# Performance work log

Measured on AMD Instinct MI355X. Metric: run time of the kernel, lower is better.

The kernel has to match this reference:

```python
import jax, jax.numpy as jnp
import numpy as np

N_BITS = 4
QN = -(2 ** (N_BITS - 1))      # -8
QP = 2 ** (N_BITS - 1) - 1     # 7

IN_F, OUT_F, RANK, N_STEPS = 4096, 4096, 8, 10


def ste_qdq(x, scale):
    """LSQ-style quantize-dequantize (forward math of STEFunction, zero_point=0)."""
    v = x / scale
    q = jnp.clip(jnp.round(v), QN, QP)
    return q * scale


def setup_inputs() -> dict:
    key = jax.random.key(0)
    ks = jax.random.split(key, 4)
    x = jax.random.normal(ks[0], (4, 2048, IN_F), dtype=jnp.float32)
    pretrained_weight = jax.random.normal(ks[1], (OUT_F, IN_F), dtype=jnp.float32)
    lora_A = jax.random.normal(ks[2], (RANK, IN_F), dtype=jnp.float32) * 0.01
    lora_B = jnp.zeros((OUT_F, RANK), dtype=jnp.float32)
    weight_scale = jnp.ones((OUT_F,), dtype=jnp.float32) * 0.1
    temporal_scales = jnp.ones((N_STEPS,), dtype=jnp.float32) * 0.1
    bias = jnp.zeros((OUT_F,), dtype=jnp.float32)
    return {
        "x": x,
        "pretrained_weight": pretrained_weight,
        "lora_A": lora_A,
        "lora_B": lora_B,
        "weight_scale": weight_scale,
        "temporal_scales": temporal_scales,
        "bias": bias,
        "current_step": 0,
    }


def reference(x, pretrained_weight, lora_A, lora_B, weight_scale, temporal_scales, bias, current_step):
    # LoRA merge: [O,R] @ [R,I] -> [O,I]
    merged_weight = pretrained_weight + lora_B @ lora_A
    # Per-out-channel weight quant (vectorized over the Python loop in the torch source)
    w_q = ste_qdq(merged_weight, weight_scale[:, None])            # [O, I]
    # Temporal activation quant with scalar scale for the current step
    x_q = ste_qdq(x, temporal_scales[current_step])                # [B, S, I]
    # F.linear: x @ W^T + b
    return jnp.einsum('bsi,oi->bso', x_q, w_q) + bias
```

## Files before the change

### kernel.cpp

```cpp
#include <hip/hip_runtime.h>
#include <stdint.h>

#define IN_F   4096
#define OUT_F  4096
#define M_ROWS 8192
#define RANK   8

typedef int v4i __attribute__((ext_vector_type(4)));

__device__ __forceinline__ int qclamp(float v, float inv) {
    float q = rintf(v * inv);
    q = fminf(fmaxf(q, -8.0f), 7.0f);
    return (int)q;
}

__device__ __forceinline__ uint32_t qpack4(float4 v, float inv) {
    uint32_t r =  (uint32_t)(qclamp(v.x, inv) & 0xFF)
               | ((uint32_t)(qclamp(v.y, inv) & 0xFF) << 8)
               | ((uint32_t)(qclamp(v.z, inv) & 0xFF) << 16)
               | ((uint32_t)(qclamp(v.w, inv) & 0xFF) << 24);
    return r;
}

__global__ __launch_bounds__(256) void quant_w_k(
    const float* __restrict__ W, const float* __restrict__ lA,
    const float* __restrict__ lB, const float* __restrict__ sw,
    uint32_t* __restrict__ qw) {
    const int t = threadIdx.x;
    const int o = blockIdx.x;
    const float inv = 1.0f / sw[o];
    float br[RANK];
#pragma unroll
    for (int r = 0; r < RANK; ++r) br[r] = lB[o * RANK + r];
    const float4* Wo = (const float4*)(W + (size_t)o * IN_F);
    const float4* A4 = (const float4*)lA;
#pragma unroll
    for (int k = 0; k < 4; ++k) {
        int i = k * 256 + t;
        float4 w = Wo[i];
#pragma unroll
        for (int r = 0; r < RANK; ++r) {
            float4 a = A4[r * 1024 + i];
            w.x = fmaf(br[r], a.x, w.x);
            w.y = fmaf(br[r], a.y, w.y);
            w.z = fmaf(br[r], a.z, w.z);
            w.w = fmaf(br[r], a.w, w.w);
        }
        qw[(size_t)o * 1024 + i] = qpack4(w, inv);
    }
}

__global__ __launch_bounds__(256) void quant_x_k(
    const float* __restrict__ x, const float* __restrict__ ts,
    const int* __restrict__ step, uint32_t* __restrict__ qx) {
    const float inv = 1.0f / ts[step[0]];
    const int t = threadIdx.x;
    const size_t base = (size_t)blockIdx.x * 1024;
#pragma unroll
    for (int k = 0; k < 4; ++k) {
        size_t i = base + k * 256 + t;
        float4 v = ((const float4*)x)[i];
        qx[i] = qpack4(v, inv);
    }
}

#define BKB 64
#define NTK (IN_F / BKB)
#define TILEB (256 * BKB)

__device__ __forceinline__ void gload16(const void* g, void* l) {
    __builtin_amdgcn_global_load_lds(
        (const __attribute__((address_space(1))) void*)g,
        (__attribute__((address_space(3))) void*)l,
        16, 0, 0);
}

__global__ __launch_bounds__(512, 2) void gemm_i8_k(
    const char* __restrict__ qx, const char* __restrict__ qw,
    const float* __restrict__ sw, const float* __restrict__ ts,
    const int* __restrict__ step, const float* __restrict__ bias,
    float* __restrict__ out) {

    __shared__ __attribute__((aligned(16))) char lsA[4][TILEB];
    __shared__ __attribute__((aligned(16))) char lsB[4][TILEB];

    const int t    = threadIdx.x;
    const int lane = t & 63;
    const int wave = t >> 6;
    const int wm   = wave >> 2;
    const int wn   = wave & 3;

    int bid = blockIdx.x;
    int swz = (bid & 7) * 64 + (bid >> 3);
    const int tn = swz & 15;
    const int tm = swz >> 4;

    const char* gA = qx + (size_t)tm * 256 * IN_F;
    const char* gB = qw + (size_t)tn * 256 * IN_F;

    auto stage_j = [&](int bb, int T, int j) {
        int i   = j * 512 + t;
        int row = i >> 2;
        int cg  = (i & 3) ^ ((row >> 1) & 3);
        size_t goff = (size_t)row * IN_F + T * BKB + cg * 16;
        gload16(gA + goff, &lsA[bb][i * 16]);
        gload16(gB + goff, &lsB[bb][i * 16]);
    };
    auto rdA = [&](int bb, int mi) -> v4i {
        int r  = wm * 128 + mi * 16 + (lane & 15);
        int pc = (lane >> 4) ^ ((r >> 1) & 3);
        return *(const v4i*)&lsA[bb][r * BKB + pc * 16];
    };
    auto rdB = [&](int bb, int ni) -> v4i {
        int r  = wn * 64 + ni * 16 + (lane & 15);
        int pc = (lane >> 4) ^ ((r >> 1) & 3);
        return *(const v4i*)&lsB[bb][r * BKB + pc * 16];
    };

    v4i acc[8][4] = {};

#pragma unroll
    for (int T0 = 0; T0 < 3; ++T0) { stage_j(T0, T0, 0); stage_j(T0, T0, 1); }

    for (int T = 0; T < NTK; ++T) {
        const int bb = T & 3;
        if (T < NTK - 2)       asm volatile("s_waitcnt vmcnt(8)" ::: "memory");
        else if (T == NTK - 2) asm volatile("s_waitcnt vmcnt(4)" ::: "memory");
        else                   asm volatile("s_waitcnt vmcnt(0)" ::: "memory");
        __builtin_amdgcn_s_barrier();

        v4i av[4], bv[4];
#pragma unroll
        for (int mi = 0; mi < 4; ++mi) av[mi] = rdA(bb, mi);
#pragma unroll
        for (int ni = 0; ni < 4; ++ni) bv[ni] = rdB(bb, ni);
        if (T + 3 < NTK) stage_j((T + 3) & 3, T + 3, 0);
        __builtin_amdgcn_s_setprio(1);
#pragma unroll
        for (int mi = 0; mi < 4; ++mi)
#pragma unroll
            for (int ni = 0; ni < 4; ++ni)
                acc[mi][ni] = __builtin_amdgcn_mfma_i32_16x16x64_i8(
                    av[mi], bv[ni], acc[mi][ni], 0, 0, 0);
        __builtin_amdgcn_s_setprio(0);

        v4i aw[4];
#pragma unroll
        for (int mi = 0; mi < 4; ++mi) aw[mi] = rdA(bb, mi + 4);
        if (T + 3 < NTK) stage_j((T + 3) & 3, T + 3, 1);
        __builtin_amdgcn_s_setprio(1);
#pragma unroll
        for (int mi = 0; mi < 4; ++mi)
#pragma unroll
            for (int ni = 0; ni < 4; ++ni)
                acc[mi + 4][ni] = __builtin_amdgcn_mfma_i32_16x16x64_i8(
                    aw[mi], bv[ni], acc[mi + 4][ni], 0, 0, 0);
        __builtin_amdgcn_s_setprio(0);
    }

    const float s_x = ts[step[0]];
#pragma unroll
    for (int ni = 0; ni < 4; ++ni) {
        int col  = tn * 256 + wn * 64 + ni * 16 + (lane & 15);
        float sc = s_x * sw[col];
        float bv = bias[col];
#pragma unroll
        for (int mi = 0; mi < 8; ++mi) {
            int row0 = tm * 256 + wm * 128 + mi * 16 + (lane >> 4) * 4;
#pragma unroll
            for (int r = 0; r < 4; ++r) {
                out[(size_t)(row0 + r) * OUT_F + col] =
                    (float)acc[mi][ni][r] * sc + bv;
            }
        }
    }
}

extern "C" void kernel_launch(void* const* d_in, const int* in_sizes, int n_in,
                              void* d_out, int out_size, void* d_ws, size_t ws_size,
                              hipStream_t stream) {
    const float* x    = (const float*)d_in[0];
    const float* W    = (const float*)d_in[1];
    const float* lA   = (const float*)d_in[2];
    const float* lB   = (const float*)d_in[3];
    const float* sw   = (const float*)d_in[4];
    const float* ts   = (const float*)d_in[5];
    const float* bias = (const float*)d_in[6];
    const int*   step = (const int*)d_in[7];
    float* out = (float*)d_out;

    char* qw = (char*)d_ws;
    char* qx = (char*)d_ws + (size_t)OUT_F * IN_F;

    quant_w_k<<<OUT_F, 256, 0, stream>>>(W, lA, lB, sw, (uint32_t*)qw);
    quant_x_k<<<M_ROWS * IN_F / 4096, 256, 0, stream>>>(x, ts, step, (uint32_t*)qx);

    gemm_i8_k<<<(M_ROWS / 256) * (OUT_F / 256), 512, 0, stream>>>(
        (const char*)qx, (const char*)qw, sw, ts, step, bias, out);
}
```

Before: 425.5 us.

## Switch int8 GEMM to 32x32x32 MFMA with restructured barrier schedule

Replaces the 16x16x64 int8 MFMA tiles with 32x32x32 int8 MFMA, changing the LDS fragment reads, accumulator layout (v16i) and epilogue row mapping. The main loop is also resynchronized with additional barriers, explicit lgkmcnt waits and sched_barriers around each half-step, and the vmcnt wait moves to after the second prefetch. Larger MFMA tiles reduce LDS read traffic per FLOP, while the extra barriers may add sync overhead.

Result: slower. 436.5 us (+2.6%).

```diff
diff --git a/kernel.cpp b/kernel.cpp
--- a/kernel.cpp
+++ b/kernel.cpp
@@ -6,7 +6,8 @@
 #define M_ROWS 8192
 #define RANK   8
 
-typedef int v4i __attribute__((ext_vector_type(4)));
+typedef int v4i  __attribute__((ext_vector_type(4)));
+typedef int v16i __attribute__((ext_vector_type(16)));
 
 __device__ __forceinline__ int qclamp(float v, float inv) {
     float q = rintf(v * inv);
@@ -64,9 +65,9 @@
     }
 }
 
-#define BKB 64
-#define NTK (IN_F / BKB)
-#define TILEB (256 * BKB)
+#define SKB   64
+#define NSK   (IN_F / SKB)
+#define SLOTB (256 * SKB)
 
 __device__ __forceinline__ void gload16(const void* g, void* l) {
     __builtin_amdgcn_global_load_lds(
@@ -81,8 +82,8 @@
     const int* __restrict__ step, const float* __restrict__ bias,
     float* __restrict__ out) {
 
-    __shared__ __attribute__((aligned(16))) char lsA[4][TILEB];
-    __shared__ __attribute__((aligned(16))) char lsB[4][TILEB];
+    __shared__ __attribute__((aligned(16))) char lsA[4][SLOTB];
+    __shared__ __attribute__((aligned(16))) char lsB[4][SLOTB];
 
     const int t    = threadIdx.x;
     const int lane = t & 63;
@@ -98,79 +99,99 @@
     const char* gA = qx + (size_t)tm * 256 * IN_F;
     const char* gB = qw + (size_t)tn * 256 * IN_F;
 
-    auto stage_j = [&](int bb, int T, int j) {
+    auto stage_j = [&](int slot, int S, int j) {
         int i   = j * 512 + t;
         int row = i >> 2;
         int cg  = (i & 3) ^ ((row >> 1) & 3);
-        size_t goff = (size_t)row * IN_F + T * BKB + cg * 16;
-        gload16(gA + goff, &lsA[bb][i * 16]);
-        gload16(gB + goff, &lsB[bb][i * 16]);
+        size_t goff = (size_t)row * IN_F + S * SKB + cg * 16;
+        gload16(gA + goff, &lsA[slot][i * 16]);
+        gload16(gB + goff, &lsB[slot][i * 16]);
     };
-    auto rdA = [&](int bb, int mi) -> v4i {
-        int r  = wm * 128 + mi * 16 + (lane & 15);
-        int pc = (lane >> 4) ^ ((r >> 1) & 3);
-        return *(const v4i*)&lsA[bb][r * BKB + pc * 16];
+    auto rdA = [&](int slot, int mf, int ks) -> v4i {
+        int r  = wm * 128 + mf * 32 + (lane & 31);
+        int pc = (ks * 2 + (lane >> 5)) ^ ((r >> 1) & 3);
+        return *(const v4i*)&lsA[slot][r * SKB + pc * 16];
     };
-    auto rdB = [&](int bb, int ni) -> v4i {
-        int r  = wn * 64 + ni * 16 + (lane & 15);
-        int pc = (lane >> 4) ^ ((r >> 1) & 3);
-        return *(const v4i*)&lsB[bb][r * BKB + pc * 16];
+    auto rdB = [&](int slot, int nf, int ks) -> v4i {
+        int r  = wn * 64 + nf * 32 + (lane & 31);
+        int pc = (ks * 2 + (lane >> 5)) ^ ((r >> 1) & 3);
+        return *(const v4i*)&lsB[slot][r * SKB + pc * 16];
     };
 
-    v4i acc[8][4] = {};
-
-#pragma unroll
-    for (int T0 = 0; T0 < 3; ++T0) { stage_j(T0, T0, 0); stage_j(T0, T0, 1); }
-
-    for (int T = 0; T < NTK; ++T) {
-        const int bb = T & 3;
-        if (T < NTK - 2)       asm volatile("s_waitcnt vmcnt(8)" ::: "memory");
-        else if (T == NTK - 2) asm volatile("s_waitcnt vmcnt(4)" ::: "memory");
-        else                   asm volatile("s_waitcnt vmcnt(0)" ::: "memory");
-        __builtin_amdgcn_s_barrier();
-
-        v4i av[4], bv[4];
-#pragma unroll
-        for (int mi = 0; mi < 4; ++mi) av[mi] = rdA(bb, mi);
-#pragma unroll
-        for (int ni = 0; ni < 4; ++ni) bv[ni] = rdB(bb, ni);
-        if (T + 3 < NTK) stage_j((T + 3) & 3, T + 3, 0);
+    v16i acc[4][2] = {};
+
+#pragma unroll
+    for (int s = 0; s < 3; ++s) { stage_j(s, s, 0); stage_j(s, s, 1); }
+    asm volatile("s_waitcnt vmcnt(8)" ::: "memory");
+    __builtin_amdgcn_s_barrier();
+
+    for (int T = 0; T < NSK; ++T) {
+        const int sl = T & 3;
+
+        v4i a0[2][2], b0[2][2];
+#pragma unroll
+        for (int mf = 0; mf < 2; ++mf)
+#pragma unroll
+            for (int ks = 0; ks < 2; ++ks) a0[mf][ks] = rdA(sl, mf, ks);
+#pragma unroll
+        for (int nf = 0; nf < 2; ++nf)
+#pragma unroll
+            for (int ks = 0; ks < 2; ++ks) b0[nf][ks] = rdB(sl, nf, ks);
+        if (T + 3 < NSK) stage_j((T + 3) & 3, T + 3, 0);
+        __builtin_amdgcn_s_barrier();
+        asm volatile("s_waitcnt lgkmcnt(0)" ::: "memory");
+        __builtin_amdgcn_sched_barrier(0);
         __builtin_amdgcn_s_setprio(1);
 #pragma unroll
-        for (int mi = 0; mi < 4; ++mi)
-#pragma unroll
-            for (int ni = 0; ni < 4; ++ni)
-                acc[mi][ni] = __builtin_amdgcn_mfma_i32_16x16x64_i8(
-                    av[mi], bv[ni], acc[mi][ni], 0, 0, 0);
+        for (int mf = 0; mf < 2; ++mf)
+#pragma unroll
+            for (int nf = 0; nf < 2; ++nf)
+#pragma unroll
+                for (int ks = 0; ks < 2; ++ks)
+                    acc[mf][nf] = __builtin_amdgcn_mfma_i32_32x32x32_i8(
+                        a0[mf][ks], b0[nf][ks], acc[mf][nf], 0, 0, 0);
         __builtin_amdgcn_s_setprio(0);
-
-        v4i aw[4];
-#pragma unroll
-        for (int mi = 0; mi < 4; ++mi) aw[mi] = rdA(bb, mi + 4);
-        if (T + 3 < NTK) stage_j((T + 3) & 3, T + 3, 1);
+        __builtin_amdgcn_s_barrier();
+
+        v4i a1[2][2];
+#pragma unroll
+        for (int mf = 0; mf < 2; ++mf)
+#pragma unroll
+            for (int ks = 0; ks < 2; ++ks) a1[mf][ks] = rdA(sl, mf + 2, ks);
+        if (T + 3 < NSK) stage_j((T + 3) & 3, T + 3, 1);
+        if (T < NSK - 3)       asm volatile("s_waitcnt vmcnt(8)" ::: "memory");
+        else if (T == NSK - 3) asm volatile("s_waitcnt vmcnt(4)" ::: "memory");
+        else if (T == NSK - 2) asm volatile("s_waitcnt vmcnt(0)" ::: "memory");
+        __builtin_amdgcn_s_barrier();
+        asm volatile("s_waitcnt lgkmcnt(0)" ::: "memory");
+        __builtin_amdgcn_sched_barrier(0);
         __builtin_amdgcn_s_setprio(1);
 #pragma unroll
-        for (int mi = 0; mi < 4; ++mi)
-#pragma unroll
-            for (int ni = 0; ni < 4; ++ni)
-                acc[mi + 4][ni] = __builtin_amdgcn_mfma_i32_16x16x64_i8(
-                    aw[mi], bv[ni], acc[mi + 4][ni], 0, 0, 0);
+        for (int mf = 0; mf < 2; ++mf)
+#pragma unroll
+            for (int nf = 0; nf < 2; ++nf)
+#pragma unroll
+                for (int ks = 0; ks < 2; ++ks)
+                    acc[mf + 2][nf] = __builtin_amdgcn_mfma_i32_32x32x32_i8(
+                        a1[mf][ks], b0[nf][ks], acc[mf + 2][nf], 0, 0, 0);
         __builtin_amdgcn_s_setprio(0);
+        __builtin_amdgcn_s_barrier();
     }
 
     const float s_x = ts[step[0]];
 #pragma unroll
-    for (int ni = 0; ni < 4; ++ni) {
-        int col  = tn * 256 + wn * 64 + ni * 16 + (lane & 15);
+    for (int nf = 0; nf < 2; ++nf) {
+        int col  = tn * 256 + wn * 64 + nf * 32 + (lane & 31);
         float sc = s_x * sw[col];
         float bv = bias[col];
 #pragma unroll
-        for (int mi = 0; mi < 8; ++mi) {
-            int row0 = tm * 256 + wm * 128 + mi * 16 + (lane >> 4) * 4;
-#pragma unroll
-            for (int r = 0; r < 4; ++r) {
-                out[(size_t)(row0 + r) * OUT_F + col] =
-                    (float)acc[mi][ni][r] * sc + bv;
+        for (int mf = 0; mf < 4; ++mf) {
+            int row_base = tm * 256 + wm * 128 + mf * 32 + (lane >> 5) * 4;
+#pragma unroll
+            for (int reg = 0; reg < 16; ++reg) {
+                int row = row_base + (reg & 3) + 8 * (reg >> 2);
+                out[(size_t)row * OUT_F + col] =
+                    (float)acc[mf][nf][reg] * sc + bv;
             }
         }
     }
```

## Double GEMM block to 16 waves with 64x64 per-wave tiles

Applied to the files above, without the earlier changes.

The int8 GEMM block grows from 512 to 1024 threads, so each of 16 waves computes a 64x64 sub-tile instead of 128x64. Each thread now stages one 16-byte chunk per K-step, and the vmcnt waits are adjusted to match. Accumulators drop from 32 to 16 v4i per thread. The goal is more resident waves per SIMD to hide LDS and global latency, at the cost of more LDS reads per MFMA (less register reuse of B fragments) and tighter register limits from launch_bounds(1024,4).

Result: no change. 419.6 us (-1.4%).

```diff
diff --git a/kernel.cpp b/kernel.cpp
--- a/kernel.cpp
+++ b/kernel.cpp
@@ -64,9 +64,9 @@
     }
 }
 
-#define BKB 64
-#define NTK (IN_F / BKB)
-#define TILEB (256 * BKB)
+#define SKB   64
+#define NSK   (IN_F / SKB)
+#define SLOTB (256 * SKB)
 
 __device__ __forceinline__ void gload16(const void* g, void* l) {
     __builtin_amdgcn_global_load_lds(
@@ -75,14 +75,14 @@
         16, 0, 0);
 }
 
-__global__ __launch_bounds__(512, 2) void gemm_i8_k(
+__global__ __launch_bounds__(1024, 4) void gemm_i8_k(
     const char* __restrict__ qx, const char* __restrict__ qw,
     const float* __restrict__ sw, const float* __restrict__ ts,
     const int* __restrict__ step, const float* __restrict__ bias,
     float* __restrict__ out) {
 
-    __shared__ __attribute__((aligned(16))) char lsA[4][TILEB];
-    __shared__ __attribute__((aligned(16))) char lsB[4][TILEB];
+    __shared__ __attribute__((aligned(16))) char lsA[4][SLOTB];
+    __shared__ __attribute__((aligned(16))) char lsB[4][SLOTB];
 
     const int t    = threadIdx.x;
     const int lane = t & 63;
@@ -98,63 +98,51 @@
     const char* gA = qx + (size_t)tm * 256 * IN_F;
     const char* gB = qw + (size_t)tn * 256 * IN_F;
 
-    auto stage_j = [&](int bb, int T, int j) {
-        int i   = j * 512 + t;
-        int row = i >> 2;
-        int cg  = (i & 3) ^ ((row >> 1) & 3);
-        size_t goff = (size_t)row * IN_F + T * BKB + cg * 16;
-        gload16(gA + goff, &lsA[bb][i * 16]);
-        gload16(gB + goff, &lsB[bb][i * 16]);
+    auto stage = [&](int slot, int S) {
+        int row = t >> 2;
+        int cg  = (t & 3) ^ ((row >> 1) & 3);
+        size_t goff = (size_t)row * IN_F + S * SKB + cg * 16;
+        gload16(gA + goff, &lsA[slot][t * 16]);
+        gload16(gB + goff, &lsB[slot][t * 16]);
     };
-    auto rdA = [&](int bb, int mi) -> v4i {
-        int r  = wm * 128 + mi * 16 + (lane & 15);
+    auto rdA = [&](int slot, int mi) -> v4i {
+        int r  = wm * 64 + mi * 16 + (lane & 15);
         int pc = (lane >> 4) ^ ((r >> 1) & 3);
-        return *(const v4i*)&lsA[bb][r * BKB + pc * 16];
+        return *(const v4i*)&lsA[slot][r * SKB + pc * 16];
     };
-    auto rdB = [&](int bb, int ni) -> v4i {
+    auto rdB = [&](int slot, int ni) -> v4i {
         int r  = wn * 64 + ni * 16 + (lane & 15);
         int pc = (lane >> 4) ^ ((r >> 1) & 3);
-        return *(const v4i*)&lsB[bb][r * BKB + pc * 16];
+        return *(const v4i*)&lsB[slot][r * SKB + pc * 16];
     };
 
-    v4i acc[8][4] = {};
+    v4i acc[4][4] = {};
 
 #pragma unroll
-    for (int T0 = 0; T0 < 3; ++T0) { stage_j(T0, T0, 0); stage_j(T0, T0, 1); }
+    for (int s = 0; s < 3; ++s) stage(s, s);
 
-    for (int T = 0; T < NTK; ++T) {
-        const int bb = T & 3;
-        if (T < NTK - 2)       asm volatile("s_waitcnt vmcnt(8)" ::: "memory");
-        else if (T == NTK - 2) asm volatile("s_waitcnt vmcnt(4)" ::: "memory");
+    for (int T = 0; T < NSK; ++T) {
+        const int sl = T & 3;
+        if (T < NSK - 2)       asm volatile("s_waitcnt vmcnt(4)" ::: "memory");
+        else if (T == NSK - 2) asm volatile("s_waitcnt vmcnt(2)" ::: "memory");
         else                   asm volatile("s_waitcnt vmcnt(0)" ::: "memory");
         __builtin_amdgcn_s_barrier();
 
-        v4i av[4], bv[4];
+        v4i a[4], b[4];
 #pragma unroll
-        for (int mi = 0; mi < 4; ++mi) av[mi] = rdA(bb, mi);
+        for (int mi = 0; mi < 4; ++mi) a[mi] = rdA(sl, mi);
 #pragma unroll
-        for (int ni = 0; ni < 4; ++ni) bv[ni] = rdB(bb, ni);
-        if (T + 3 < NTK) stage_j((T + 3) & 3, T + 3, 0);
+        for (int ni = 0; ni < 4; ++ni) b[ni] = rdB(sl, ni);
+
+        if (T + 3 < NSK) stage((T + 3) & 3, T + 3);
+
         __builtin_amdgcn_s_setprio(1);
 #pragma unroll
         for (int mi = 0; mi < 4; ++mi)
 #pragma unroll
             for (int ni = 0; ni < 4; ++ni)
                 acc[mi][ni] = __builtin_amdgcn_mfma_i32_16x16x64_i8(
-                    av[mi], bv[ni], acc[mi][ni], 0, 0, 0);
-        __builtin_amdgcn_s_setprio(0);
-
-        v4i aw[4];
-#pragma unroll
-        for (int mi = 0; mi < 4; ++mi) aw[mi] = rdA(bb, mi + 4);
-        if (T + 3 < NTK) stage_j((T + 3) & 3, T + 3, 1);
-        __builtin_amdgcn_s_setprio(1);
-#pragma unroll
-        for (int mi = 0; mi < 4; ++mi)
-#pragma unroll
-            for (int ni = 0; ni < 4; ++ni)
-                acc[mi + 4][ni] = __builtin_amdgcn_mfma_i32_16x16x64_i8(
-                    aw[mi], bv[ni], acc[mi + 4][ni], 0, 0, 0);
+                    a[mi], b[ni], acc[mi][ni], 0, 0, 0);
         __builtin_amdgcn_s_setprio(0);
     }
 
@@ -165,8 +153,8 @@
         float sc = s_x * sw[col];
         float bv = bias[col];
 #pragma unroll
-        for (int mi = 0; mi < 8; ++mi) {
-            int row0 = tm * 256 + wm * 128 + mi * 16 + (lane >> 4) * 4;
+        for (int mi = 0; mi < 4; ++mi) {
+            int row0 = tm * 256 + wm * 64 + mi * 16 + (lane >> 4) * 4;
 #pragma unroll
             for (int r = 0; r < 4; ++r) {
                 out[(size_t)(row0 + r) * OUT_F + col] =
@@ -195,6 +183,6 @@
     quant_w_k<<<OUT_F, 256, 0, stream>>>(W, lA, lB, sw, (uint32_t*)qw);
     quant_x_k<<<M_ROWS * IN_F / 4096, 256, 0, stream>>>(x, ts, step, (uint32_t*)qx);
 
-    gemm_i8_k<<<(M_ROWS / 256) * (OUT_F / 256), 512, 0, stream>>>(
+    gemm_i8_k<<<(M_ROWS / 256) * (OUT_F / 256), 1024, 0, stream>>>(
         (const char*)qx, (const char*)qw, sw, ts, step, bias, out);
 }
```
